# Kernel optimization log

Hardware: AMD Instinct MI355X
Metric: run time of the kernel (lower is better)

Reference implementation:

```python
import jax, jax.numpy as jnp
import numpy as np

EMB = 1024
HEADS = EMB // 64  # 16, head_dim = 64


def setup_inputs() -> dict:
    key = jax.random.key(0)
    ks = jax.random.split(key, 9)
    a, m, t, e = 4, 2048, 2048, EMB
    s = 1.0 / np.sqrt(e)
    return {
        "q": jax.random.normal(ks[0], (a, m, e), jnp.float32),
        "k": jax.random.normal(ks[1], (a, t, e), jnp.float32),
        "v": jax.random.normal(ks[2], (a, t, e), jnp.float32),
        "Wq": jax.random.normal(ks[3], (e, e), jnp.float32) * s,
        "bq": jnp.zeros((e,), jnp.float32),
        "Wk": jax.random.normal(ks[4], (e, e), jnp.float32) * s,
        "bk": jnp.zeros((e,), jnp.float32),
        "Wv": jax.random.normal(ks[5], (e, e), jnp.float32) * s,
        "bv": jnp.zeros((e,), jnp.float32),
    }


def reference(q, k, v, Wq, bq, Wk, bk, Wv, bv):
    a, m, e = q.shape
    t = k.shape[1]
    h = HEADS
    # linear projections (torch Linear: x @ W.T + b)
    qp = (q @ Wq.T + bq).reshape(a, m, h, -1).transpose(0, 2, 1, 3)  # [a,h,m,c]
    kp = (k @ Wk.T + bk).reshape(a, t, h, -1).transpose(0, 2, 1, 3)  # [a,h,t,c]
    vp = (v @ Wv.T + bv).reshape(a, t, h, -1).transpose(0, 2, 1, 3)  # [a,h,t,c]
    # NOTE: original forward never applies self.scale — unscaled QK^T (faithful)
    dots = jnp.einsum('ahmc,ahtc->ahmt', qp, kp)
    attn = jax.nn.softmax(dots, axis=-1)
    out = jnp.einsum('ahmt,ahtc->ahmc', attn, vp)
    return out.transpose(0, 2, 1, 3).reshape(a, m, e)
```

## Files before the change

kernel.cpp:

```cpp
#include <hip/hip_runtime.h>
#include <hip/hip_bf16.h>
#include <hip/hip_fp16.h>

using half8  = __attribute__((ext_vector_type(8))) _Float16;
using float4v = __attribute__((ext_vector_type(4))) float;
using f32x16 = __attribute__((ext_vector_type(16))) float;
typedef unsigned int uint;

#define A_DIM 4
#define M_DIM 2048
#define E_DIM 1024
#define H_DIM 16
#define C_DIM 64
#define PLANE (M_DIM * C_DIM)
#define PROJ_ELEMS (A_DIM * H_DIM * PLANE)
#define LOG2E 1.44269504088896f

#define GLOAD_LDS16(g, l) __builtin_amdgcn_global_load_lds( \
    (const __attribute__((address_space(1))) void*)(g), \
    (__attribute__((address_space(3))) void*)(l), 16, 0, 0)

#if __has_builtin(__builtin_amdgcn_exp2f)
#define EXP2F(x) __builtin_amdgcn_exp2f(x)
#else
#define EXP2F(x) exp2f(x)
#endif

static __device__ __forceinline__ uint pk16(float a, float b) {
    auto r = __builtin_amdgcn_cvt_pkrtz(a, b);
    return __builtin_bit_cast(uint, r);
}

static __device__ __forceinline__ half8 ldsfrag_cvt32(const float* base, int row, int gb) {
    const char* b = (const char*)base;
    int off = row * 128 + (gb ^ ((row & 7) << 4));
    float4v x0 = *reinterpret_cast<const float4v*>(b + off);
    float4v x1 = *reinterpret_cast<const float4v*>(b + (off ^ 16));
    union { uint u[4]; half8 v; } r;
    r.u[0] = pk16(x0[0], x0[1]);
    r.u[1] = pk16(x0[2], x0[3]);
    r.u[2] = pk16(x1[0], x1[1]);
    r.u[3] = pk16(x1[2], x1[3]);
    return r.v;
}

__global__ __launch_bounds__(256, 2)
void proj_kernel(const float* __restrict__ q, const float* __restrict__ k,
                 const float* __restrict__ v,
                 const float* __restrict__ Wq, const float* __restrict__ Wk,
                 const float* __restrict__ Wv,
                 const float* __restrict__ bq, const float* __restrict__ bk,
                 const float* __restrict__ bv,
                 _Float16* __restrict__ qp, _Float16* __restrict__ kp,
                 _Float16* __restrict__ vt)
{
    __shared__ float ldsA[2][128 * 32];
    __shared__ float ldsB[2][128 * 32];

    const int z = blockIdx.y;
    const float* X    = (z == 0) ? q  : (z == 1) ? k  : v;
    const float* W    = (z == 0) ? Wq : (z == 1) ? Wk : Wv;
    const float* bias = (z == 0) ? bq : (z == 1) ? bk : bv;
    _Float16* out     = (z == 0) ? qp : (z == 1) ? kp : vt;
    const bool TR = (z == 2);

    const int bid = blockIdx.x;
    const int xcd = bid & 7;
    const int idx = bid >> 3;
    const int R0 = (xcd * 8 + (idx >> 3)) * 128;
    const int C0 = (idx & 7) * 128;

    const int tid  = threadIdx.x;
    const int lane = tid & 63;
    const int wave = tid >> 6;
    const int wr = wave >> 1, wc = wave & 1;
    const int g = lane >> 4, r16 = lane & 15;

    auto stage = [&](int buf, int k0) {
#pragma unroll
        for (int i = 0; i < 4; i++) {
            int seg  = i * 256 + tid;
            int row  = seg >> 3;
            int swzo = ((seg & 7) * 16) ^ ((row & 7) << 4);
            const char* asrc = (const char*)&X[(size_t)(R0 + row) * E_DIM + k0] + swzo;
            const char* bsrc = (const char*)&W[(size_t)(C0 + row) * E_DIM + k0] + swzo;
            GLOAD_LDS16(asrc, &ldsA[buf][seg * 4]);
            GLOAD_LDS16(bsrc, &ldsB[buf][seg * 4]);
        }
    };

    float4v acc[4][4];
#pragma unroll
    for (int i = 0; i < 4; i++)
#pragma unroll
        for (int j = 0; j < 4; j++) acc[i][j] = {0.f, 0.f, 0.f, 0.f};

    stage(0, 0);

    for (int it = 0; it < E_DIM / 32; ++it) {
        __syncthreads();
        if (it + 1 < E_DIM / 32) stage((it + 1) & 1, (it + 1) * 32);
        const float* A = ldsA[it & 1];
        const float* B = ldsB[it & 1];

        half8 af[4], bf[4];
#pragma unroll
        for (int mi = 0; mi < 4; mi++)
            af[mi] = ldsfrag_cvt32(A, wr * 64 + mi * 16 + r16, g * 32);
#pragma unroll
        for (int ni = 0; ni < 4; ni++)
            bf[ni] = ldsfrag_cvt32(B, wc * 64 + ni * 16 + r16, g * 32);
#pragma unroll
        for (int mi = 0; mi < 4; mi++)
#pragma unroll
            for (int ni = 0; ni < 4; ni++)
                acc[mi][ni] = __builtin_amdgcn_mfma_f32_16x16x32_f16(af[mi], bf[ni], acc[mi][ni], 0, 0, 0);
    }

#pragma unroll
    for (int mi = 0; mi < 4; mi++) {
#pragma unroll
        for (int ni = 0; ni < 4; ni++) {
            const int jb = C0 + wc * 64 + ni * 16 + r16;
            const int h  = jb >> 6;
            const int cc = jb & 63;
            const float bv = bias[jb];
            if (!TR) {
#pragma unroll
                for (int reg = 0; reg < 4; reg++) {
                    int b = R0 + wr * 64 + mi * 16 + g * 4 + reg;
                    float val = acc[mi][ni][reg] + bv;
                    size_t o = (size_t)((b >> 11) * H_DIM + h) * PLANE + (size_t)(b & (M_DIM - 1)) * C_DIM + cc;
                    out[o] = (_Float16)val;
                }
            } else {
                int b0 = R0 + wr * 64 + mi * 16 + g * 4;
                uint u0 = pk16(acc[mi][ni][0] + bv, acc[mi][ni][1] + bv);
                uint u1 = pk16(acc[mi][ni][2] + bv, acc[mi][ni][3] + bv);
                size_t o = (size_t)((b0 >> 11) * H_DIM + h) * PLANE + (size_t)cc * M_DIM + (b0 & (M_DIM - 1));
                *reinterpret_cast<uint*>(&out[o]) = u0;
                *reinterpret_cast<uint*>(&out[o] + 2) = u1;
            }
        }
    }
}

__global__ __launch_bounds__(256, 4)
void flash_kernel(const _Float16* __restrict__ qp, const _Float16* __restrict__ kp,
                  const _Float16* __restrict__ vt, float* __restrict__ out)
{
    __shared__ _Float16 smem[2][2][4096];

    const int tid  = threadIdx.x;
    const int lane = tid & 63;
    const int wave = tid >> 6;
    const int l31  = lane & 31;
    const int hi   = lane >> 5;

    const int bid = blockIdx.x;
    const int wg  = ((bid & 7) << 7) | (bid >> 3);
    const int plane_i = wg >> 4;
    const int qt      = wg & 15;
    const size_t plane = (size_t)plane_i * PLANE;
    const int q0 = qt * 128 + wave * 32;

    const int srow  = tid >> 3;
    const int lincb = (tid & 7) * 16;
    const int scb   = lincb ^ ((srow & 7) << 4);

    half8 qf[4];
#pragma unroll
    for (int ch = 0; ch < 4; ch++)
        qf[ch] = *reinterpret_cast<const half8*>(&qp[plane + (size_t)(q0 + l31) * C_DIM + ch * 16 + hi * 8]);

    f32x16 o0, o1;
#pragma unroll
    for (int i = 0; i < 16; i++) { o0[i] = 0.f; o1[i] = 0.f; }
    float m = -INFINITY, l = 0.f;

    auto stage = [&](int buf, int t0) {
#pragma unroll
        for (int i = 0; i < 2; i++) {
            int row = srow + 32 * i;
            const char* ksrc = (const char*)&kp[plane + (size_t)(t0 + row) * C_DIM] + scb;
            const char* vsrc = (const char*)&vt[plane + (size_t)row * M_DIM + t0] + scb;
            GLOAD_LDS16(ksrc, &smem[buf][0][tid * 8 + 2048 * i]);
            GLOAD_LDS16(vsrc, &smem[buf][1][tid * 8 + 2048 * i]);
        }
    };

    stage(0, 0);

    for (int it = 0; it < M_DIM / 64; ++it) {
        __syncthreads();
        if (it + 1 < M_DIM / 64) stage((it + 1) & 1, (it + 1) * 64);
        const int cur = it & 1;
        const char* kbase = (const char*)smem[cur][0];
        const char* vbase = (const char*)smem[cur][1];

#pragma unroll
        for (int st = 0; st < 2; ++st) {
            const int krow = st * 32 + l31;
            const int kswz = (krow & 7) << 4;
            f32x16 s;
#pragma unroll
            for (int i = 0; i < 16; i++) s[i] = 0.f;
            __builtin_amdgcn_s_setprio(1);
#pragma unroll
            for (int ch = 0; ch < 4; ch++) {
                int cb = (ch * 32 + hi * 16) ^ kswz;
                half8 kf = *reinterpret_cast<const half8*>(kbase + krow * 128 + cb);
                s = __builtin_amdgcn_mfma_f32_32x32x16_f16(kf, qf[ch], s, 0, 0, 0);
            }
            __builtin_amdgcn_s_setprio(0);

            float a0 = fmaxf(fmaxf(s[0],  s[1]),  s[2]);
            float a1 = fmaxf(fmaxf(s[3],  s[4]),  s[5]);
            float a2 = fmaxf(fmaxf(s[6],  s[7]),  s[8]);
            float a3 = fmaxf(fmaxf(s[9],  s[10]), s[11]);
            float a4 = fmaxf(fmaxf(s[12], s[13]), s[14]);
            float pm = fmaxf(fmaxf(fmaxf(a0, a1), a2),
                             fmaxf(fmaxf(a3, a4), s[15]));
            pm = fmaxf(pm, __shfl_xor(pm, 32));
            if (!__all(pm <= m + 8.f)) {
                float mnew = fmaxf(m, pm);
                float sc = EXP2F((m - mnew) * LOG2E);
                m = mnew; l *= sc;
                o0 *= sc; o1 *= sc;
            }
            const float mK = m * LOG2E;
            float p[16];
#pragma unroll
            for (int r = 0; r < 16; r++) p[r] = EXP2F(fmaf(s[r], LOG2E, -mK));
            float t0a = (p[0] + p[1]) + (p[2] + p[3]);
            float t1a = (p[4] + p[5]) + (p[6] + p[7]);
            float t2a = (p[8] + p[9]) + (p[10] + p[11]);
            float t3a = (p[12] + p[13]) + (p[14] + p[15]);
            l += (t0a + t1a) + (t2a + t3a);

            half8 pf[2];
#pragma unroll
            for (int c0 = 0; c0 < 2; c0++) {
                uint ua0 = pk16(p[8 * c0 + 0], p[8 * c0 + 1]);
                uint ua1 = pk16(p[8 * c0 + 2], p[8 * c0 + 3]);
                uint ub0 = pk16(p[8 * c0 + 4], p[8 * c0 + 5]);
                uint ub1 = pk16(p[8 * c0 + 6], p[8 * c0 + 7]);
                uint v0 = hi ? ua0 : ub0;
                uint v1 = hi ? ua1 : ub1;
                uint y0 = (uint)__shfl_xor((int)v0, 32);
                uint y1 = (uint)__shfl_xor((int)v1, 32);
                union { uint u[4]; half8 v; } pu;
                pu.u[0] = hi ? y0 : ua0;
                pu.u[1] = hi ? y1 : ua1;
                pu.u[2] = hi ? ub0 : y0;
                pu.u[3] = hi ? ub1 : y1;
                pf[c0] = pu.v;
            }

            __builtin_amdgcn_s_setprio(1);
#pragma unroll
            for (int db = 0; db < 2; db++) {
                const int vrow = db * 32 + l31;
                const int vswz = (vrow & 7) << 4;
#pragma unroll
                for (int c0 = 0; c0 < 2; c0++) {
                    int cb = (st * 64 + c0 * 32 + hi * 16) ^ vswz;
                    half8 vf = *reinterpret_cast<const half8*>(vbase + vrow * 128 + cb);
                    if (db == 0) o0 = __builtin_amdgcn_mfma_f32_32x32x16_f16(vf, pf[c0], o0, 0, 0, 0);
                    else         o1 = __builtin_amdgcn_mfma_f32_32x32x16_f16(vf, pf[c0], o1, 0, 0, 0);
                }
            }
            __builtin_amdgcn_s_setprio(0);
        }
    }

    const int aa = plane_i >> 4;
    const int hh = plane_i & 15;
    const float lt = l + __shfl_xor(l, 32);
    const float inv = 1.f / lt;
    float* obase = out + ((size_t)(aa * M_DIM + q0 + l31)) * E_DIM + hh * C_DIM;
#pragma unroll
    for (int db = 0; db < 2; db++) {
#pragma unroll
        for (int g4 = 0; g4 < 4; g4++) {
            float4v w;
#pragma unroll
            for (int j = 0; j < 4; j++) w[j] = (db ? o1[4 * g4 + j] : o0[4 * g4 + j]) * inv;
            int d0 = db * 32 + 8 * g4 + 4 * hi;
            *reinterpret_cast<float4v*>(obase + d0) = w;
        }
    }
}

extern "C" void kernel_launch(void* const* d_in, const int* in_sizes, int n_in,
                              void* d_out, int out_size, void* d_ws, size_t ws_size,
                              hipStream_t stream)
{
    const float* q  = (const float*)d_in[0];
    const float* k  = (const float*)d_in[1];
    const float* v  = (const float*)d_in[2];
    const float* Wq = (const float*)d_in[3];
    const float* bq = (const float*)d_in[4];
    const float* Wk = (const float*)d_in[5];
    const float* bk = (const float*)d_in[6];
    const float* Wv = (const float*)d_in[7];
    const float* bv = (const float*)d_in[8];
    float* out = (float*)d_out;

    _Float16* qp = (_Float16*)d_ws;
    _Float16* kp = qp + PROJ_ELEMS;
    _Float16* vt = kp + PROJ_ELEMS;

    hipLaunchKernelGGL(proj_kernel, dim3(512, 3), dim3(256), 0, stream,
                       q, k, v, Wq, Wk, Wv, bq, bk, bv, qp, kp, vt);
    hipLaunchKernelGGL(flash_kernel, dim3(A_DIM * H_DIM * (M_DIM / 128)), dim3(256), 0, stream, qp, kp, vt, out);
}
```

Baseline: 212.0 us.

## Stage projection GEMM tiles as fp16 in LDS via register prefetch

The projection GEMM no longer copies fp32 tiles straight into LDS with global_load_lds and converts them on every fragment read. Each thread now loads the fp32 tile into registers, converts it to fp16 once, and writes padded fp16 rows to LDS. This halves LDS footprint and read traffic, and the launch bound rises to 4 blocks per CU. In exchange it adds register pressure and needs a manual wait and barrier, and global load latency now sits in registers across the MFMA loop.

```diff
diff --git a/kernel.cpp b/kernel.cpp
--- a/kernel.cpp
+++ b/kernel.cpp
@@ -31,20 +31,7 @@
     return __builtin_bit_cast(uint, r);
 }
 
-static __device__ __forceinline__ half8 ldsfrag_cvt32(const float* base, int row, int gb) {
-    const char* b = (const char*)base;
-    int off = row * 128 + (gb ^ ((row & 7) << 4));
-    float4v x0 = *reinterpret_cast<const float4v*>(b + off);
-    float4v x1 = *reinterpret_cast<const float4v*>(b + (off ^ 16));
-    union { uint u[4]; half8 v; } r;
-    r.u[0] = pk16(x0[0], x0[1]);
-    r.u[1] = pk16(x0[2], x0[3]);
-    r.u[2] = pk16(x1[0], x1[1]);
-    r.u[3] = pk16(x1[2], x1[3]);
-    return r.v;
-}
-
-__global__ __launch_bounds__(256, 2)
+__global__ __launch_bounds__(256, 4)
 void proj_kernel(const float* __restrict__ q, const float* __restrict__ k,
                  const float* __restrict__ v,
                  const float* __restrict__ Wq, const float* __restrict__ Wk,
@@ -54,8 +41,8 @@
                  _Float16* __restrict__ qp, _Float16* __restrict__ kp,
                  _Float16* __restrict__ vt)
 {
-    __shared__ float ldsA[2][128 * 32];
-    __shared__ float ldsB[2][128 * 32];
+    __shared__ _Float16 ldsA[2][128 * 40];
+    __shared__ _Float16 ldsB[2][128 * 40];
 
     const int z = blockIdx.y;
     const float* X    = (z == 0) ? q  : (z == 1) ? k  : v;
@@ -76,18 +63,40 @@
     const int wr = wave >> 1, wc = wave & 1;
     const int g = lane >> 4, r16 = lane & 15;
 
-    auto stage = [&](int buf, int k0) {
+    const int srow  = tid >> 1;
+    const int shalf = tid & 1;
+    const float* aptr = &X[(size_t)(R0 + srow) * E_DIM + shalf * 16];
+    const float* bptr = &W[(size_t)(C0 + srow) * E_DIM + shalf * 16];
+    const int wbyte = srow * 80 + shalf * 32;
+
+    float4v ra[4], rb[4];
+    auto gload = [&](int k0) {
 #pragma unroll
         for (int i = 0; i < 4; i++) {
-            int seg  = i * 256 + tid;
-            int row  = seg >> 3;
-            int swzo = ((seg & 7) * 16) ^ ((row & 7) << 4);
-            const char* asrc = (const char*)&X[(size_t)(R0 + row) * E_DIM + k0] + swzo;
-            const char* bsrc = (const char*)&W[(size_t)(C0 + row) * E_DIM + k0] + swzo;
-            GLOAD_LDS16(asrc, &ldsA[buf][seg * 4]);
-            GLOAD_LDS16(bsrc, &ldsB[buf][seg * 4]);
+            ra[i] = *reinterpret_cast<const float4v*>(aptr + k0 + i * 4);
+            rb[i] = *reinterpret_cast<const float4v*>(bptr + k0 + i * 4);
         }
     };
+    auto dswrite = [&](int buf) {
+        union { uint u[4]; half8 h; } c0a, c1a, c0b, c1b;
+#pragma unroll
+        for (int i = 0; i < 2; i++) {
+            c0a.u[2*i]   = pk16(ra[i][0], ra[i][1]);
+            c0a.u[2*i+1] = pk16(ra[i][2], ra[i][3]);
+            c1a.u[2*i]   = pk16(ra[2+i][0], ra[2+i][1]);
+            c1a.u[2*i+1] = pk16(ra[2+i][2], ra[2+i][3]);
+            c0b.u[2*i]   = pk16(rb[i][0], rb[i][1]);
+            c0b.u[2*i+1] = pk16(rb[i][2], rb[i][3]);
+            c1b.u[2*i]   = pk16(rb[2+i][0], rb[2+i][1]);
+            c1b.u[2*i+1] = pk16(rb[2+i][2], rb[2+i][3]);
+        }
+        char* pa = (char*)ldsA[buf] + wbyte;
+        char* pb = (char*)ldsB[buf] + wbyte;
+        *reinterpret_cast<half8*>(pa)      = c0a.h;
+        *reinterpret_cast<half8*>(pa + 16) = c1a.h;
+        *reinterpret_cast<half8*>(pb)      = c0b.h;
+        *reinterpret_cast<half8*>(pb + 16) = c1b.h;
+    };
 
     float4v acc[4][4];
 #pragma unroll
@@ -95,26 +104,37 @@
 #pragma unroll
         for (int j = 0; j < 4; j++) acc[i][j] = {0.f, 0.f, 0.f, 0.f};
 
-    stage(0, 0);
-
+    gload(0);
+    dswrite(0);
+    asm volatile("s_waitcnt lgkmcnt(0)" ::: "memory");
+    __builtin_amdgcn_s_barrier();
+
+    int cur = 0;
     for (int it = 0; it < E_DIM / 32; ++it) {
-        __syncthreads();
-        if (it + 1 < E_DIM / 32) stage((it + 1) & 1, (it + 1) * 32);
-        const float* A = ldsA[it & 1];
-        const float* B = ldsB[it & 1];
-
+        const bool more = (it + 1 < E_DIM / 32);
+        if (more) gload((it + 1) * 32);
+
+        const char* Ab = (const char*)ldsA[cur];
+        const char* Bb = (const char*)ldsB[cur];
         half8 af[4], bf[4];
 #pragma unroll
         for (int mi = 0; mi < 4; mi++)
-            af[mi] = ldsfrag_cvt32(A, wr * 64 + mi * 16 + r16, g * 32);
+            af[mi] = *reinterpret_cast<const half8*>(Ab + (wr * 64 + mi * 16 + r16) * 80 + g * 16);
 #pragma unroll
         for (int ni = 0; ni < 4; ni++)
-            bf[ni] = ldsfrag_cvt32(B, wc * 64 + ni * 16 + r16, g * 32);
+            bf[ni] = *reinterpret_cast<const half8*>(Bb + (wc * 64 + ni * 16 + r16) * 80 + g * 16);
 #pragma unroll
         for (int mi = 0; mi < 4; mi++)
 #pragma unroll
             for (int ni = 0; ni < 4; ni++)
                 acc[mi][ni] = __builtin_amdgcn_mfma_f32_16x16x32_f16(af[mi], bf[ni], acc[mi][ni], 0, 0, 0);
+
+        if (more) {
+            dswrite(cur ^ 1);
+            asm volatile("s_waitcnt lgkmcnt(0)" ::: "memory");
+            __builtin_amdgcn_s_barrier();
+            cur ^= 1;
+        }
     }
 
 #pragma unroll
```

Result: slower. 227.9 us (+7.5%).
